# Kernel optimization log

Hardware: AMD Instinct MI355X
Metric: run time of the kernel (lower is better)

Reference implementation:

```python
import jax, jax.numpy as jnp
import numpy as np

N = 8192
D_IN = 128
D_OUT = 64


def setup_inputs() -> dict:
    key = jax.random.key(0)
    k1, k2, k3 = jax.random.split(key, 3)
    features = jax.random.normal(k1, (N, D_IN), dtype=jnp.float32)
    # uniform [0,1) entries -> strictly positive row sums (degrees)
    adjacency_matrix = jax.random.uniform(k2, (N, N), dtype=jnp.float32)
    weight = jax.random.normal(k3, (D_IN, D_OUT), dtype=jnp.float32)
    return {"features": features, "adjacency_matrix": adjacency_matrix, "weight": weight}


def reference(features, adjacency_matrix, weight):
    # degree_matrix = diag(rowsum(A)); inverse(sqrt(diag(d))) == diag(d^{-1/2})
    deg = jnp.sum(adjacency_matrix, axis=1)            # [N]
    d_inv_sqrt = 1.0 / jnp.sqrt(deg)                   # [N]
    # D^{-1/2} A D^{-1/2} via broadcasting instead of dense diag matmuls
    norm_adj = d_inv_sqrt[:, None] * adjacency_matrix * d_inv_sqrt[None, :]  # [N,N]
    # (norm_adj @ X) @ W -- contract small dim last for efficiency
    h = norm_adj @ features                            # [N, D_IN]
    return jax.nn.relu(h @ weight)                     # [N, D_OUT]
```

## Files before the change

### kernel.cpp

```cpp
#include <hip/hip_runtime.h>

#define N_NODES 8192
#define D_IN    128
#define D_OUT   64
#define NSPLIT  8

typedef __attribute__((ext_vector_type(8))) short short8;
typedef __attribute__((ext_vector_type(4))) float f32x4;

__device__ __forceinline__ short f2bf(float f) {
    unsigned u = __builtin_bit_cast(unsigned, f);
    u += 0x7fff + ((u >> 16) & 1);
    return (short)(u >> 16);
}

__global__ __launch_bounds__(256) void k_degpack(const float* __restrict__ A,
                                                 float* __restrict__ deg,
                                                 unsigned short* __restrict__ Ap) {
    const int tid = threadIdx.x;
    const int r = tid >> 4, c = tid & 15;
    const int ri = blockIdx.x;
    const int row = ri * 16 + r;
    const f32x4* Ar = (const f32x4*)(A + (size_t)row * N_NODES + c * 8);
    short8* Apv = (short8*)Ap;
    const size_t ubase = ((size_t)ri * 256 + (c >> 2)) * 64 + (c & 3) * 16 + r;

    float s = 0.f;
    f32x4 a0 = __builtin_nontemporal_load(Ar);
    f32x4 a1 = __builtin_nontemporal_load(Ar + 1);
#pragma unroll 4
    for (int m = 0; m < 64; ++m) {
        f32x4 b0, b1;
        if (m < 63) {
            b0 = __builtin_nontemporal_load(Ar + (m + 1) * 32);
            b1 = __builtin_nontemporal_load(Ar + (m + 1) * 32 + 1);
        }
        s += (a0[0] + a0[1]) + (a0[2] + a0[3]) + (a1[0] + a1[1]) + (a1[2] + a1[3]);
        short8 p;
        p[0] = f2bf(a0[0]); p[1] = f2bf(a0[1]); p[2] = f2bf(a0[2]); p[3] = f2bf(a0[3]);
        p[4] = f2bf(a1[0]); p[5] = f2bf(a1[1]); p[6] = f2bf(a1[2]); p[7] = f2bf(a1[3]);
        Apv[ubase + (size_t)m * 256] = p;
        a0 = b0; a1 = b1;
    }
#pragma unroll
    for (int off = 1; off < 16; off <<= 1) s += __shfl_xor(s, off, 64);
    if (c == 0) deg[row] = s;
}

__global__ __launch_bounds__(256) void k_spmm_bf16(const unsigned short* __restrict__ Ap,
                                                   const unsigned short* __restrict__ Gp,
                                                   float* __restrict__ h2s) {
    const int lane = threadIdx.x & 63;
    const int wave = threadIdx.x >> 6;
    const int quad = lane >> 4;
    const int l15  = lane & 15;
    const int ri   = blockIdx.x * 4 + wave;
    const int kt0  = blockIdx.y * 32;

    const short8* Af = (const short8*)Ap + ((size_t)ri * 256 + kt0) * 64 + lane;
    const short8* Gq = (const short8*)Gp + (size_t)kt0 * 256 + lane;

    f32x4 acc[4] = {};
#pragma unroll 2
    for (int i = 0; i < 32; ++i) {
        short8 af = Af[i * 64];
        const short8* gb = Gq + i * 256;
#pragma unroll
        for (int u = 0; u < 4; ++u) {
            acc[u] = __builtin_amdgcn_mfma_f32_16x16x32_bf16(af, gb[u * 64], acc[u], 0, 0, 0);
        }
    }
    float* H = h2s + (size_t)blockIdx.y * ((size_t)N_NODES * D_OUT);
    const int r0 = ri * 16 + quad * 4;
#pragma unroll
    for (int u = 0; u < 4; ++u)
#pragma unroll
        for (int r = 0; r < 4; ++r)
            H[(size_t)(r0 + r) * D_OUT + u * 16 + l15] = acc[u][r];
}

__global__ __launch_bounds__(256) void k_gpack(const float* __restrict__ X,
                                               const float* __restrict__ W,
                                               const float* __restrict__ deg,
                                               unsigned short* __restrict__ Gp) {
    __shared__ float Wl[D_IN * D_OUT];
    __shared__ float Xl[32 * 129];
    const int t = blockIdx.x, tid = threadIdx.x;

    const float4* W4 = (const float4*)W;
    float4* Wl4 = (float4*)Wl;
#pragma unroll
    for (int i = 0; i < 8; ++i) Wl4[tid + 256 * i] = W4[tid + 256 * i];
    const float4* X4 = (const float4*)(X + (size_t)t * 32 * D_IN);
#pragma unroll
    for (int i = 0; i < 4; ++i) {
        int idx = tid + 256 * i;
        float4 v = X4[idx];
        int r = idx >> 5, c = (idx & 31) * 4;
        float* dst = Xl + r * 129 + c;
        dst[0] = v.x; dst[1] = v.y; dst[2] = v.z; dst[3] = v.w;
    }
    __syncthreads();

    const int kl = tid & 31;
    const int nb = (tid >> 5) * 8;
    float acc[8] = {0.f, 0.f, 0.f, 0.f, 0.f, 0.f, 0.f, 0.f};
    const float* xr = Xl + kl * 129;
    for (int d = 0; d < D_IN; ++d) {
        float xv = xr[d];
        const float* wr = Wl + d * D_OUT + nb;
#pragma unroll
        for (int c = 0; c < 8; ++c) acc[c] += xv * wr[c];
    }
    const float scale = rsqrtf(deg[t * 32 + kl]);
    const int quad = kl >> 3, j = kl & 7;
#pragma unroll
    for (int c = 0; c < 8; ++c) {
        int n = nb + c;
        int u = n >> 4;
        int lanei = quad * 16 + (n & 15);
        Gp[(((size_t)t * 4 + u) * 64 + lanei) * 8 + j] = (unsigned short)f2bf(acc[c] * scale);
    }
}

__global__ __launch_bounds__(256) void k_out(const float* __restrict__ h2s,
                                             const float* __restrict__ deg,
                                             float* __restrict__ out) {
    const int idx = blockIdx.x * 256 + threadIdx.x;
    const f32x4* H = (const f32x4*)h2s;
    const int slice = N_NODES * D_OUT / 4;
    f32x4 s = H[idx];
#pragma unroll
    for (int p = 1; p < NSPLIT; ++p) s += H[idx + (size_t)p * slice];
    const float sc = rsqrtf(deg[idx >> 4]);
    f32x4 o;
#pragma unroll
    for (int c = 0; c < 4; ++c) o[c] = fmaxf(s[c] * sc, 0.f);
    ((f32x4*)out)[idx] = o;
}

__global__ __launch_bounds__(256) void k_deg(const float* __restrict__ A,
                                             float* __restrict__ deg) {
    const int wave = threadIdx.x >> 6;
    const int lane = threadIdx.x & 63;
    const int row  = blockIdx.x * 4 + wave;
    const float4* Ar = (const float4*)(A + (size_t)row * N_NODES);
    float s = 0.f;
#pragma unroll
    for (int i = 0; i < 32; ++i) {
        float4 v = Ar[lane + 64 * i];
        s += (v.x + v.y) + (v.z + v.w);
    }
#pragma unroll
    for (int off = 32; off; off >>= 1) s += __shfl_down(s, off, 64);
    if (lane == 0) deg[row] = s;
}

__global__ __launch_bounds__(256) void k_spmm_f32(const float* __restrict__ A,
                                                  const unsigned short* __restrict__ Gp,
                                                  float* __restrict__ h2s) {
    const int lane = threadIdx.x & 63;
    const int wave = threadIdx.x >> 6;
    const int quad = lane >> 4;
    const int l15  = lane & 15;
    const int row  = blockIdx.x * 64 + wave * 16 + l15;
    const float* Ar = A + (size_t)row * N_NODES;
    const int kt0 = blockIdx.y * 32;

    f32x4 acc[4] = {};
    const short8* Gq = (const short8*)Gp;

    for (int kt = kt0; kt < kt0 + 32; ++kt) {
        const float4* pa = (const float4*)(Ar + kt * 32 + quad * 8);
        float4 a0 = pa[0], a1 = pa[1];
        short8 af;
        af[0] = f2bf(a0.x); af[1] = f2bf(a0.y); af[2] = f2bf(a0.z); af[3] = f2bf(a0.w);
        af[4] = f2bf(a1.x); af[5] = f2bf(a1.y); af[6] = f2bf(a1.z); af[7] = f2bf(a1.w);
        const short8* gb = Gq + (size_t)kt * 4 * 64 + lane;
#pragma unroll
        for (int u = 0; u < 4; ++u) {
            acc[u] = __builtin_amdgcn_mfma_f32_16x16x32_bf16(af, gb[u * 64], acc[u], 0, 0, 0);
        }
    }
    float* H = h2s + (size_t)blockIdx.y * ((size_t)N_NODES * D_OUT);
    const int r0 = blockIdx.x * 64 + wave * 16 + quad * 4;
#pragma unroll
    for (int u = 0; u < 4; ++u)
#pragma unroll
        for (int r = 0; r < 4; ++r)
            H[(size_t)(r0 + r) * D_OUT + u * 16 + l15] = acc[u][r];
}

extern "C" void kernel_launch(void* const* d_in, const int* in_sizes, int n_in,
                              void* d_out, int out_size, void* d_ws, size_t ws_size,
                              hipStream_t stream) {
    const float* X = (const float*)d_in[0];
    const float* A = (const float*)d_in[1];
    const float* W = (const float*)d_in[2];
    float* out = (float*)d_out;

    char* ws = (char*)d_ws;
    float*          deg = (float*)ws;
    unsigned short* Gp  = (unsigned short*)(ws + 32768);
    float*          h2s = (float*)(ws + 32768 + 1048576);
    unsigned short* Ap  = (unsigned short*)(ws + 32768 + 1048576 + 16777216);

    const size_t need = 32768 + 1048576 + 16777216 + (size_t)N_NODES * N_NODES * 2;

    if (ws_size >= need) {
        k_degpack<<<N_NODES / 16, 256, 0, stream>>>(A, deg, Ap);
        k_gpack  <<<N_NODES / 32, 256, 0, stream>>>(X, W, deg, Gp);
        k_spmm_bf16<<<dim3(N_NODES / 64, NSPLIT), 256, 0, stream>>>(Ap, Gp, h2s);
        k_out    <<<(N_NODES * D_OUT / 4) / 256, 256, 0, stream>>>(h2s, deg, out);
    } else {
        k_deg    <<<N_NODES / 4, 256, 0, stream>>>(A, deg);
        k_gpack  <<<N_NODES / 32, 256, 0, stream>>>(X, W, deg, Gp);
        k_spmm_f32<<<dim3(N_NODES / 64, NSPLIT), 256, 0, stream>>>(A, Gp, h2s);
        k_out    <<<(N_NODES * D_OUT / 4) / 256, 256, 0, stream>>>(h2s, deg, out);
    }
}
```

Before: 411.0 us.

## Fuse split-K reduction and ReLU epilogue into bf16 SpMM kernel

Replaces the 8-way split-K bf16 SpMM plus separate k_out reduction with one kernel per 16-row block. Each of the four waves handles a quarter of K, partial sums are reduced through shared memory, and the kernel applies the degree scaling and ReLU before writing the output directly. This removes the 16MB partial-sum buffer and its write and read traffic, and drops one kernel launch. In exchange the grid has fewer, longer blocks (512 blocks each streaming 16 rows of A), which may reduce memory-level parallelism.

```diff
diff --git a/kernel.cpp b/kernel.cpp
--- a/kernel.cpp
+++ b/kernel.cpp
@@ -47,38 +47,6 @@
     if (c == 0) deg[row] = s;
 }
 
-__global__ __launch_bounds__(256) void k_spmm_bf16(const unsigned short* __restrict__ Ap,
-                                                   const unsigned short* __restrict__ Gp,
-                                                   float* __restrict__ h2s) {
-    const int lane = threadIdx.x & 63;
-    const int wave = threadIdx.x >> 6;
-    const int quad = lane >> 4;
-    const int l15  = lane & 15;
-    const int ri   = blockIdx.x * 4 + wave;
-    const int kt0  = blockIdx.y * 32;
-
-    const short8* Af = (const short8*)Ap + ((size_t)ri * 256 + kt0) * 64 + lane;
-    const short8* Gq = (const short8*)Gp + (size_t)kt0 * 256 + lane;
-
-    f32x4 acc[4] = {};
-#pragma unroll 2
-    for (int i = 0; i < 32; ++i) {
-        short8 af = Af[i * 64];
-        const short8* gb = Gq + i * 256;
-#pragma unroll
-        for (int u = 0; u < 4; ++u) {
-            acc[u] = __builtin_amdgcn_mfma_f32_16x16x32_bf16(af, gb[u * 64], acc[u], 0, 0, 0);
-        }
-    }
-    float* H = h2s + (size_t)blockIdx.y * ((size_t)N_NODES * D_OUT);
-    const int r0 = ri * 16 + quad * 4;
-#pragma unroll
-    for (int u = 0; u < 4; ++u)
-#pragma unroll
-        for (int r = 0; r < 4; ++r)
-            H[(size_t)(r0 + r) * D_OUT + u * 16 + l15] = acc[u][r];
-}
-
 __global__ __launch_bounds__(256) void k_gpack(const float* __restrict__ X,
                                                const float* __restrict__ W,
                                                const float* __restrict__ deg,
@@ -123,20 +91,46 @@
     }
 }
 
-__global__ __launch_bounds__(256) void k_out(const float* __restrict__ h2s,
-                                             const float* __restrict__ deg,
-                                             float* __restrict__ out) {
-    const int idx = blockIdx.x * 256 + threadIdx.x;
-    const f32x4* H = (const f32x4*)h2s;
-    const int slice = N_NODES * D_OUT / 4;
-    f32x4 s = H[idx];
-#pragma unroll
-    for (int p = 1; p < NSPLIT; ++p) s += H[idx + (size_t)p * slice];
-    const float sc = rsqrtf(deg[idx >> 4]);
-    f32x4 o;
-#pragma unroll
-    for (int c = 0; c < 4; ++c) o[c] = fmaxf(s[c] * sc, 0.f);
-    ((f32x4*)out)[idx] = o;
+__global__ __launch_bounds__(256) void k_spmm_fused(const unsigned short* __restrict__ Ap,
+                                                    const unsigned short* __restrict__ Gp,
+                                                    const float* __restrict__ deg,
+                                                    float* __restrict__ out) {
+    __shared__ f32x4 lds[256 * 4];
+    const int lane = threadIdx.x & 63;
+    const int wave = threadIdx.x >> 6;
+    const int quad = lane >> 4;
+    const int l15  = lane & 15;
+    const int ri   = blockIdx.x;
+    const int kt0  = wave * 64;
+
+    const short8* Af = (const short8*)Ap + ((size_t)ri * 256 + kt0) * 64 + lane;
+    const short8* Gq = (const short8*)Gp + (size_t)kt0 * 256 + lane;
+
+    f32x4 acc[4] = {};
+#pragma unroll 4
+    for (int i = 0; i < 64; ++i) {
+        short8 af = Af[i * 64];
+        const short8* gb = Gq + i * 256;
+#pragma unroll
+        for (int u = 0; u < 4; ++u) {
+            acc[u] = __builtin_amdgcn_mfma_f32_16x16x32_bf16(af, gb[u * 64], acc[u], 0, 0, 0);
+        }
+    }
+#pragma unroll
+    for (int u = 0; u < 4; ++u) lds[(wave * 64 + lane) * 4 + u] = acc[u];
+    __syncthreads();
+
+    f32x4 v = lds[lane * 4 + wave];
+#pragma unroll
+    for (int wp = 1; wp < 4; ++wp) v += lds[(wp * 64 + lane) * 4 + wave];
+
+    const f32x4 d4 = *(const f32x4*)(deg + ri * 16 + quad * 4);
+#pragma unroll
+    for (int r = 0; r < 4; ++r) {
+        const float sc = rsqrtf(d4[r]);
+        out[(size_t)(ri * 16 + quad * 4 + r) * D_OUT + wave * 16 + l15] =
+            fmaxf(v[r] * sc, 0.f);
+    }
 }
 
 __global__ __launch_bounds__(256) void k_deg(const float* __restrict__ A,
@@ -191,6 +185,22 @@
             H[(size_t)(r0 + r) * D_OUT + u * 16 + l15] = acc[u][r];
 }
 
+__global__ __launch_bounds__(256) void k_out(const float* __restrict__ h2s,
+                                             const float* __restrict__ deg,
+                                             float* __restrict__ out) {
+    const int idx = blockIdx.x * 256 + threadIdx.x;
+    const f32x4* H = (const f32x4*)h2s;
+    const int slice = N_NODES * D_OUT / 4;
+    f32x4 s = H[idx];
+#pragma unroll
+    for (int p = 1; p < NSPLIT; ++p) s += H[idx + (size_t)p * slice];
+    const float sc = rsqrtf(deg[idx >> 4]);
+    f32x4 o;
+#pragma unroll
+    for (int c = 0; c < 4; ++c) o[c] = fmaxf(s[c] * sc, 0.f);
+    ((f32x4*)out)[idx] = o;
+}
+
 extern "C" void kernel_launch(void* const* d_in, const int* in_sizes, int n_in,
                               void* d_out, int out_size, void* d_ws, size_t ws_size,
                               hipStream_t stream) {
@@ -202,20 +212,19 @@
     char* ws = (char*)d_ws;
     float*          deg = (float*)ws;
     unsigned short* Gp  = (unsigned short*)(ws + 32768);
+    unsigned short* Ap  = (unsigned short*)(ws + 32768 + 1048576);
     float*          h2s = (float*)(ws + 32768 + 1048576);
-    unsigned short* Ap  = (unsigned short*)(ws + 32768 + 1048576 + 16777216);
-
-    const size_t need = 32768 + 1048576 + 16777216 + (size_t)N_NODES * N_NODES * 2;
-
-    if (ws_size >= need) {
-        k_degpack<<<N_NODES / 16, 256, 0, stream>>>(A, deg, Ap);
-        k_gpack  <<<N_NODES / 32, 256, 0, stream>>>(X, W, deg, Gp);
-        k_spmm_bf16<<<dim3(N_NODES / 64, NSPLIT), 256, 0, stream>>>(Ap, Gp, h2s);
-        k_out    <<<(N_NODES * D_OUT / 4) / 256, 256, 0, stream>>>(h2s, deg, out);
+
+    const size_t need_fused = 32768 + 1048576 + (size_t)N_NODES * N_NODES * 2;
+
+    if (ws_size >= need_fused) {
+        k_degpack   <<<N_NODES / 16, 256, 0, stream>>>(A, deg, Ap);
+        k_gpack     <<<N_NODES / 32, 256, 0, stream>>>(X, W, deg, Gp);
+        k_spmm_fused<<<N_NODES / 16, 256, 0, stream>>>(Ap, Gp, deg, out);
     } else {
-        k_deg    <<<N_NODES / 4, 256, 0, stream>>>(A, deg);
-        k_gpack  <<<N_NODES / 32, 256, 0, stream>>>(X, W, deg, Gp);
+        k_deg     <<<N_NODES / 4, 256, 0, stream>>>(A, deg);
+        k_gpack   <<<N_NODES / 32, 256, 0, stream>>>(X, W, deg, Gp);
         k_spmm_f32<<<dim3(N_NODES / 64, NSPLIT), 256, 0, stream>>>(A, Gp, h2s);
-        k_out    <<<(N_NODES * D_OUT / 4) / 256, 256, 0, stream>>>(h2s, deg, out);
-    }
-}
+        k_out     <<<(N_NODES * D_OUT / 4) / 256, 256, 0, stream>>>(h2s, deg, out);
+    }
+}
```

After: 421.8 us. +2.6%, slower.
